# Kernel optimization log

Hardware: AMD Instinct MI355X
Metric: run time of the kernel (lower is better)

The kernel has to match this reference:

```python
import jax, jax.numpy as jnp
import numpy as np

VOCAB = 50257
EMBED_DIM = 768
NUM_TUNE = 1024


def setup_inputs() -> dict:
    key = jax.random.key(0)
    k_ids, k_tune, k_base, k_train = jax.random.split(key, 4)
    input_ids = jax.random.randint(k_ids, (8, 4096), 0, VOCAB, dtype=jnp.int64)
    tune_ids = jnp.sort(jax.random.randint(k_tune, (NUM_TUNE,), 0, VOCAB, dtype=jnp.int64))
    base_weight = jax.random.normal(k_base, (VOCAB, EMBED_DIM), dtype=jnp.float32)
    # In the torch module train_weight is initialized from base rows; independent init is fine for a numeric baseline.
    train_weight = jax.random.normal(k_train, (NUM_TUNE, EMBED_DIM), dtype=jnp.float32)
    return {"input_ids": input_ids, "tune_ids": tune_ids,
            "base_weight": base_weight, "train_weight": train_weight}


def reference(input_ids, tune_ids, base_weight, train_weight):
    # Precompute id -> train-row mapping (replaces the torch.isin + python-loop dict lookup).
    id2row = jnp.full((VOCAB,), -1, dtype=jnp.int32)
    id2row = id2row.at[tune_ids].set(jnp.arange(NUM_TUNE, dtype=jnp.int32))
    out = base_weight[input_ids]                      # [B, S, D] gather
    rows = id2row[input_ids]                          # [B, S] train-row index or -1
    mask = rows >= 0
    override = train_weight[jnp.maximum(rows, 0)]     # [B, S, D]
    return jnp.where(mask[..., None], override, out)
```

## Files before the change

kernel.cpp:

```cpp
#include <hip/hip_runtime.h>


#define EMBED_DIM 768
#define EMBED_DIM4 (EMBED_DIM / 4)
#define WAVES_PER_BLOCK 4
#define BLOCK_THREADS (WAVES_PER_BLOCK * 64)
#define NUM_TUNE_C 1024

typedef __attribute__((ext_vector_type(4))) float f4;

__global__ __launch_bounds__(BLOCK_THREADS) void split_embedding_kernel(
    const int* __restrict__ input_ids,
    const int* __restrict__ tune_ids,
    const float* __restrict__ base_weight,
    const float* __restrict__ train_weight,
    float* __restrict__ out,
    int num_tokens, int num_tune)
{
    const int wave  = threadIdx.x >> 6;
    const int lane  = threadIdx.x & 63;
    const int token = blockIdx.x * WAVES_PER_BLOCK + wave;
    if (token >= num_tokens) return;

    const int tok = input_ids[token];

    int cand = -1;
    int cval = -1;

    if (num_tune == NUM_TUNE_C) {
        const int v1 = tune_ids[lane << 4];
        const unsigned long long b1 = __ballot(v1 <= tok);
        const int seg = __popcll(b1) - 1;
        if (seg >= 0) {
            const int v2 = tune_ids[(seg << 4) + (lane & 15)];
            const unsigned long long b2 = __ballot(v2 <= tok) & 0xFFFFull;
            const int cnt = __popcll(b2);
            cand = (seg << 4) + cnt - 1;
            cval = __shfl(v2, cand & 15);
        }
    } else {
        int lo = 0, hi = num_tune;
        while (lo < hi) {
            const int mid = (lo + hi) >> 1;
            if (tune_ids[mid] <= tok) lo = mid + 1;
            else                      hi = mid;
        }
        cand = lo - 1;
        if (cand >= 0) cval = tune_ids[cand];
    }

    const f4* src;
    if (cand >= 0 && cval == tok) {
        src = (const f4*)(train_weight + (size_t)cand * EMBED_DIM);
    } else {
        src = (const f4*)(base_weight + (size_t)tok * EMBED_DIM);
    }
    f4* dst = (f4*)(out + (size_t)token * EMBED_DIM);

    f4 r0 = src[lane];
    f4 r1 = src[lane + 64];
    f4 r2 = src[lane + 128];
    __builtin_nontemporal_store(r0, dst + lane);
    __builtin_nontemporal_store(r1, dst + lane + 64);
    __builtin_nontemporal_store(r2, dst + lane + 128);
}

extern "C" void kernel_launch(void* const* d_in, const int* in_sizes, int n_in,
                              void* d_out, int out_size, void* d_ws, size_t ws_size,
                              hipStream_t stream) {
    const int*   input_ids    = (const int*)d_in[0];
    const int*   tune_ids     = (const int*)d_in[1];
    const float* base_weight  = (const float*)d_in[2];
    const float* train_weight = (const float*)d_in[3];
    float*       out          = (float*)d_out;

    const int num_tokens = in_sizes[0];
    const int num_tune   = in_sizes[1];

    const int grid = (num_tokens + WAVES_PER_BLOCK - 1) / WAVES_PER_BLOCK;
    split_embedding_kernel<<<grid, BLOCK_THREADS, 0, stream>>>(
        input_ids, tune_ids, base_weight, train_weight, out, num_tokens, num_tune);
}
```

Measured before the change: 242.8 us.

## Prefetch base rows speculatively, process two tokens per wave, stage tune ids in LDS

Each wave now handles two tokens and issues the base-weight row loads before the tune-id search, overwriting them with train-weight rows only when a match is found. The tune-id table is staged into shared memory once per block, and the block size grows to eight waves. This is meant to hide the search latency behind the row fetch and raise memory-level parallelism. The cost is a block-wide barrier and some redundant base-row reads for tuned tokens, which are rare.

```diff
diff --git a/kernel.cpp b/kernel.cpp
--- a/kernel.cpp
+++ b/kernel.cpp
@@ -2,12 +2,14 @@
 
 
 #define EMBED_DIM 768
-#define EMBED_DIM4 (EMBED_DIM / 4)
-#define WAVES_PER_BLOCK 4
+#define WAVES_PER_BLOCK 8
 #define BLOCK_THREADS (WAVES_PER_BLOCK * 64)
+#define TOKENS_PER_WAVE 2
+#define TOKENS_PER_BLOCK (WAVES_PER_BLOCK * TOKENS_PER_WAVE)
 #define NUM_TUNE_C 1024
 
 typedef __attribute__((ext_vector_type(4))) float f4;
+typedef __attribute__((ext_vector_type(4))) int   i4;
 
 __global__ __launch_bounds__(BLOCK_THREADS) void split_embedding_kernel(
     const int* __restrict__ input_ids,
@@ -17,52 +19,105 @@
     float* __restrict__ out,
     int num_tokens, int num_tune)
 {
-    const int wave  = threadIdx.x >> 6;
-    const int lane  = threadIdx.x & 63;
-    const int token = blockIdx.x * WAVES_PER_BLOCK + wave;
-    if (token >= num_tokens) return;
+    __shared__ int lds_tune[NUM_TUNE_C];
+    __shared__ int lds_heads[64];
 
-    const int tok = input_ids[token];
+    const int wave = threadIdx.x >> 6;
+    const int lane = threadIdx.x & 63;
+    const int tokenA = blockIdx.x * TOKENS_PER_BLOCK + wave * TOKENS_PER_WAVE;
+    const int tokenB = tokenA + 1;
 
-    int cand = -1;
-    int cval = -1;
+    const bool vA = (tokenA < num_tokens);
+    const bool vB = (tokenB < num_tokens);
+
+    const int tokA = vA ? input_ids[tokenA] : 0;
+    const int tokB = vB ? input_ids[tokenB] : 0;
+
+    const f4* __restrict__ srcA = (const f4*)(base_weight + (size_t)tokA * EMBED_DIM);
+    const f4* __restrict__ srcB = (const f4*)(base_weight + (size_t)tokB * EMBED_DIM);
+    f4 a0, a1, a2, b0, b1, b2;
+    if (vA) { a0 = srcA[lane]; a1 = srcA[lane + 64]; a2 = srcA[lane + 128]; }
+    if (vB) { b0 = srcB[lane]; b1 = srcB[lane + 64]; b2 = srcB[lane + 128]; }
+
+    int candA = -1, cvalA = -1;
+    int candB = -1, cvalB = -1;
 
     if (num_tune == NUM_TUNE_C) {
-        const int v1 = tune_ids[lane << 4];
-        const unsigned long long b1 = __ballot(v1 <= tok);
-        const int seg = __popcll(b1) - 1;
-        if (seg >= 0) {
-            const int v2 = tune_ids[(seg << 4) + (lane & 15)];
-            const unsigned long long b2 = __ballot(v2 <= tok) & 0xFFFFull;
-            const int cnt = __popcll(b2);
-            cand = (seg << 4) + cnt - 1;
-            cval = __shfl(v2, cand & 15);
+        if (threadIdx.x < NUM_TUNE_C / 4) {
+            const i4 v = ((const i4*)tune_ids)[threadIdx.x];
+            *(i4*)&lds_tune[threadIdx.x * 4] = v;
+            if ((threadIdx.x & 3) == 0) lds_heads[threadIdx.x >> 2] = v.x;
+        }
+        __syncthreads();
+
+        {
+            const int v1 = lds_heads[lane];
+            const unsigned long long b1 = __ballot(v1 <= tokA);
+            const int seg = __popcll(b1) - 1;
+            if (seg >= 0) {
+                const int v2 = lds_tune[(seg << 4) + (lane & 15)];
+                const unsigned long long b2 = __ballot(v2 <= tokA) & 0xFFFFull;
+                const int cnt = __popcll(b2);
+                candA = (seg << 4) + cnt - 1;
+                cvalA = __shfl(v2, candA & 15);
+            }
+        }
+        {
+            const int v1 = lds_heads[lane];
+            const unsigned long long b1 = __ballot(v1 <= tokB);
+            const int seg = __popcll(b1) - 1;
+            if (seg >= 0) {
+                const int v2 = lds_tune[(seg << 4) + (lane & 15)];
+                const unsigned long long b2 = __ballot(v2 <= tokB) & 0xFFFFull;
+                const int cnt = __popcll(b2);
+                candB = (seg << 4) + cnt - 1;
+                cvalB = __shfl(v2, candB & 15);
+            }
         }
     } else {
-        int lo = 0, hi = num_tune;
-        while (lo < hi) {
-            const int mid = (lo + hi) >> 1;
-            if (tune_ids[mid] <= tok) lo = mid + 1;
-            else                      hi = mid;
+        if (vA) {
+            int lo = 0, hi = num_tune;
+            while (lo < hi) {
+                const int mid = (lo + hi) >> 1;
+                if (tune_ids[mid] <= tokA) lo = mid + 1;
+                else                       hi = mid;
+            }
+            candA = lo - 1;
+            if (candA >= 0) cvalA = tune_ids[candA];
         }
-        cand = lo - 1;
-        if (cand >= 0) cval = tune_ids[cand];
+        if (vB) {
+            int lo = 0, hi = num_tune;
+            while (lo < hi) {
+                const int mid = (lo + hi) >> 1;
+                if (tune_ids[mid] <= tokB) lo = mid + 1;
+                else                       hi = mid;
+            }
+            candB = lo - 1;
+            if (candB >= 0) cvalB = tune_ids[candB];
+        }
     }
 
-    const f4* src;
-    if (cand >= 0 && cval == tok) {
-        src = (const f4*)(train_weight + (size_t)cand * EMBED_DIM);
-    } else {
-        src = (const f4*)(base_weight + (size_t)tok * EMBED_DIM);
+    if (vA && candA >= 0 && cvalA == tokA) {
+        const f4* t = (const f4*)(train_weight + (size_t)candA * EMBED_DIM);
+        a0 = t[lane]; a1 = t[lane + 64]; a2 = t[lane + 128];
     }
-    f4* dst = (f4*)(out + (size_t)token * EMBED_DIM);
+    if (vB && candB >= 0 && cvalB == tokB) {
+        const f4* t = (const f4*)(train_weight + (size_t)candB * EMBED_DIM);
+        b0 = t[lane]; b1 = t[lane + 64]; b2 = t[lane + 128];
+    }
 
-    f4 r0 = src[lane];
-    f4 r1 = src[lane + 64];
-    f4 r2 = src[lane + 128];
-    __builtin_nontemporal_store(r0, dst + lane);
-    __builtin_nontemporal_store(r1, dst + lane + 64);
-    __builtin_nontemporal_store(r2, dst + lane + 128);
+    f4* dstA = (f4*)(out + (size_t)tokenA * EMBED_DIM);
+    f4* dstB = (f4*)(out + (size_t)tokenB * EMBED_DIM);
+    if (vA) {
+        __builtin_nontemporal_store(a0, dstA + lane);
+        __builtin_nontemporal_store(a1, dstA + lane + 64);
+        __builtin_nontemporal_store(a2, dstA + lane + 128);
+    }
+    if (vB) {
+        __builtin_nontemporal_store(b0, dstB + lane);
+        __builtin_nontemporal_store(b1, dstB + lane + 64);
+        __builtin_nontemporal_store(b2, dstB + lane + 128);
+    }
 }
 
 extern "C" void kernel_launch(void* const* d_in, const int* in_sizes, int n_in,
@@ -77,7 +132,7 @@
     const int num_tokens = in_sizes[0];
     const int num_tune   = in_sizes[1];
 
-    const int grid = (num_tokens + WAVES_PER_BLOCK - 1) / WAVES_PER_BLOCK;
+    const int grid = (num_tokens + TOKENS_PER_BLOCK - 1) / TOKENS_PER_BLOCK;
     split_embedding_kernel<<<grid, BLOCK_THREADS, 0, stream>>>(
         input_ids, tune_ids, base_weight, train_weight, out, num_tokens, num_tune);
 }
```

Result: no change. 242.0 us (-0.3%).

## Process four tokens per wave with LDS-staged tune_ids search

Applied to the files above, without the earlier changes.

Each wave now handles four tokens instead of one, with block size doubled to eight waves. The tune_ids table is staged into shared memory once per block, so the two-level ballot search reads LDS instead of global memory. All four rows are loaded before any store is issued. The aim is more memory-level parallelism per wave and less per-token search overhead, at the cost of more registers, a block-wide barrier, and fewer blocks in the grid.

```diff
diff --git a/kernel.cpp b/kernel.cpp
--- a/kernel.cpp
+++ b/kernel.cpp
@@ -2,12 +2,14 @@
 
 
 #define EMBED_DIM 768
-#define EMBED_DIM4 (EMBED_DIM / 4)
-#define WAVES_PER_BLOCK 4
+#define WAVES_PER_BLOCK 8
 #define BLOCK_THREADS (WAVES_PER_BLOCK * 64)
+#define TPW 4
+#define TOKENS_PER_BLOCK (WAVES_PER_BLOCK * TPW)
 #define NUM_TUNE_C 1024
 
 typedef __attribute__((ext_vector_type(4))) float f4;
+typedef __attribute__((ext_vector_type(4))) int   i4;
 
 __global__ __launch_bounds__(BLOCK_THREADS) void split_embedding_kernel(
     const int* __restrict__ input_ids,
@@ -17,52 +19,93 @@
     float* __restrict__ out,
     int num_tokens, int num_tune)
 {
+    __shared__ int lds_tune[NUM_TUNE_C];
+    __shared__ int lds_heads[64];
+
     const int wave  = threadIdx.x >> 6;
     const int lane  = threadIdx.x & 63;
-    const int token = blockIdx.x * WAVES_PER_BLOCK + wave;
-    if (token >= num_tokens) return;
+    const int tbase = blockIdx.x * TOKENS_PER_BLOCK + wave * TPW;
 
-    const int tok = input_ids[token];
+    int  toks[TPW];
+    bool valid[TPW];
+    if (tbase + TPW <= num_tokens) {
+        const i4 t4 = *(const i4*)(input_ids + tbase);
+        toks[0] = t4.x; toks[1] = t4.y; toks[2] = t4.z; toks[3] = t4.w;
+        valid[0] = valid[1] = valid[2] = valid[3] = true;
+    } else {
+        #pragma unroll
+        for (int t = 0; t < TPW; ++t) {
+            valid[t] = (tbase + t < num_tokens);
+            toks[t]  = valid[t] ? input_ids[tbase + t] : 0;
+        }
+    }
 
-    int cand = -1;
-    int cval = -1;
+    const float* src[TPW];
 
     if (num_tune == NUM_TUNE_C) {
-        const int v1 = tune_ids[lane << 4];
-        const unsigned long long b1 = __ballot(v1 <= tok);
-        const int seg = __popcll(b1) - 1;
-        if (seg >= 0) {
-            const int v2 = tune_ids[(seg << 4) + (lane & 15)];
-            const unsigned long long b2 = __ballot(v2 <= tok) & 0xFFFFull;
-            const int cnt = __popcll(b2);
-            cand = (seg << 4) + cnt - 1;
-            cval = __shfl(v2, cand & 15);
+        if (threadIdx.x < NUM_TUNE_C / 4) {
+            const i4 v = ((const i4*)tune_ids)[threadIdx.x];
+            *(i4*)&lds_tune[threadIdx.x * 4] = v;
+            if ((threadIdx.x & 3) == 0) lds_heads[threadIdx.x >> 2] = v.x;
+        }
+        __syncthreads();
+
+        const int h = lds_heads[lane];
+
+        #pragma unroll
+        for (int t = 0; t < TPW; ++t) {
+            const int tok = toks[t];
+            const unsigned long long b1 = __ballot(h <= tok);
+            const int seg = __popcll(b1) - 1;
+            const float* s = base_weight + (size_t)tok * EMBED_DIM;
+            if (seg >= 0) {
+                const int v2 = lds_tune[(seg << 4) + (lane & 15)];
+                const unsigned long long b2 = __ballot(v2 <= tok) & 0xFFFFull;
+                const int cand = (seg << 4) + __popcll(b2) - 1;
+                const int cval = __shfl(v2, cand & 15);
+                if (cval == tok)
+                    s = train_weight + (size_t)cand * EMBED_DIM;
+            }
+            src[t] = s;
         }
     } else {
-        int lo = 0, hi = num_tune;
-        while (lo < hi) {
-            const int mid = (lo + hi) >> 1;
-            if (tune_ids[mid] <= tok) lo = mid + 1;
-            else                      hi = mid;
+        #pragma unroll
+        for (int t = 0; t < TPW; ++t) {
+            const int tok = toks[t];
+            int lo = 0, hi = num_tune;
+            while (lo < hi) {
+                const int mid = (lo + hi) >> 1;
+                if (tune_ids[mid] <= tok) lo = mid + 1;
+                else                      hi = mid;
+            }
+            const int cand = lo - 1;
+            const float* s = base_weight + (size_t)tok * EMBED_DIM;
+            if (cand >= 0 && tune_ids[cand] == tok)
+                s = train_weight + (size_t)cand * EMBED_DIM;
+            src[t] = s;
         }
-        cand = lo - 1;
-        if (cand >= 0) cval = tune_ids[cand];
     }
 
-    const f4* src;
-    if (cand >= 0 && cval == tok) {
-        src = (const f4*)(train_weight + (size_t)cand * EMBED_DIM);
-    } else {
-        src = (const f4*)(base_weight + (size_t)tok * EMBED_DIM);
+    f4 r[TPW][3];
+    #pragma unroll
+    for (int t = 0; t < TPW; ++t) {
+        if (valid[t]) {
+            const f4* s4 = (const f4*)src[t];
+            r[t][0] = s4[lane];
+            r[t][1] = s4[lane + 64];
+            r[t][2] = s4[lane + 128];
+        }
     }
-    f4* dst = (f4*)(out + (size_t)token * EMBED_DIM);
 
-    f4 r0 = src[lane];
-    f4 r1 = src[lane + 64];
-    f4 r2 = src[lane + 128];
-    __builtin_nontemporal_store(r0, dst + lane);
-    __builtin_nontemporal_store(r1, dst + lane + 64);
-    __builtin_nontemporal_store(r2, dst + lane + 128);
+    #pragma unroll
+    for (int t = 0; t < TPW; ++t) {
+        if (valid[t]) {
+            f4* d4 = (f4*)(out + (size_t)(tbase + t) * EMBED_DIM);
+            __builtin_nontemporal_store(r[t][0], d4 + lane);
+            __builtin_nontemporal_store(r[t][1], d4 + lane + 64);
+            __builtin_nontemporal_store(r[t][2], d4 + lane + 128);
+        }
+    }
 }
 
 extern "C" void kernel_launch(void* const* d_in, const int* in_sizes, int n_in,
@@ -77,7 +120,7 @@
     const int num_tokens = in_sizes[0];
     const int num_tune   = in_sizes[1];
 
-    const int grid = (num_tokens + WAVES_PER_BLOCK - 1) / WAVES_PER_BLOCK;
+    const int grid = (num_tokens + TOKENS_PER_BLOCK - 1) / TOKENS_PER_BLOCK;
     split_embedding_kernel<<<grid, BLOCK_THREADS, 0, stream>>>(
         input_ids, tune_ids, base_weight, train_weight, out, num_tokens, num_tune);
 }
```

New measurement: 244.3 us. About the same (+0.6%).
